# Optimization experiments

Hardware: AMD Instinct MI355X
Metric: run time of the kernel (lower is better)

## Reference

```python
import jax, jax.numpy as jnp
import numpy as np

B, P, H = 256, 20, 4  # images, boxes per image, humans per image
F, L, S, HD, C = 1024, 300, 16, 1024, 117

def _build_edges():
    s, d = np.meshgrid(np.arange(P), np.arange(P), indexing='ij')
    m = s != d
    src_l, dst_l = s[m], d[m]  # 380 fully-connected edges per image (src-major order)
    eid_tab = -np.ones((P, P), np.int64)
    eid_tab[src_l, dst_l] = np.arange(src_l.shape[0])
    rs, rd = np.meshgrid(np.arange(P), np.arange(H), indexing='ij')
    rm = rs != rd
    r_eid = eid_tab[rs[rm], rd[rm]]  # 76 readout edges per image (human dst)
    off_n = (np.arange(B) * P)[:, None]
    off_e = (np.arange(B) * src_l.shape[0])[:, None]
    edge_src = (src_l[None] + off_n).ravel().astype(np.int32)
    edge_dst = (dst_l[None] + off_n).ravel().astype(np.int32)
    readout_eid = (r_eid[None] + off_e).ravel().astype(np.int32)
    return edge_src, edge_dst, readout_eid

def setup_inputs() -> dict:
    key = jax.random.key(0)
    ks = jax.random.split(key, 12)
    es, ed, re = _build_edges()
    N = B * P
    D_in = 2 * F + 2 * L + S  # 2664
    return {
        'feat': jax.random.normal(ks[0], (N, F), jnp.float32),
        'word2vec': jax.random.normal(ks[1], (N, L), jnp.float32),
        'spatial_feat': jax.random.normal(ks[2], (es.shape[0], S), jnp.float32),
        'W_v': jax.random.normal(ks[3], (F, F), jnp.float32) / np.float32(np.sqrt(F)),
        'a_v': jax.random.normal(ks[4], (2 * F,), jnp.float32) * 0.05,
        'W_l': jax.random.normal(ks[5], (L, L), jnp.float32) / np.float32(np.sqrt(L)),
        'a_l': jax.random.normal(ks[6], (2 * L,), jnp.float32) * 0.05,
        'W1': jax.random.normal(ks[7], (D_in, HD), jnp.float32) / np.float32(np.sqrt(D_in)),
        'b1': jnp.zeros((HD,), jnp.float32),
        'W2': jax.random.normal(ks[8], (HD, C), jnp.float32) / np.float32(np.sqrt(HD)),
        'b2': jnp.zeros((C,), jnp.float32),
        'edge_src': jnp.asarray(es),
        'edge_dst': jnp.asarray(ed),
        'readout_eid': jnp.asarray(re),
    }

def _gat_update(x, W, a, src, dst, n):
    # graph-attention message passing (GRNN step): attention over incoming edges per dst
    h = x @ W                      # [N, d]
    d = h.shape[1]
    e_src = h @ a[:d]              # [N]
    e_dst = h @ a[d:]
    e = jax.nn.leaky_relu(e_src[src] + e_dst[dst], 0.2)          # [E]
    emax = jax.ops.segment_max(e, dst, num_segments=n)
    ee = jnp.exp(e - emax[dst])
    denom = jax.ops.segment_sum(ee, dst, num_segments=n)
    alpha = ee / (denom[dst] + 1e-9)                              # segment softmax
    msg = jax.ops.segment_sum(alpha[:, None] * h[src], dst, num_segments=n)  # [N, d]
    return jax.nn.relu(x + msg)

def reference(feat, word2vec, spatial_feat, W_v, a_v, W_l, a_l, W1, b1, W2, b2,
              edge_src, edge_dst, readout_eid):
    n = feat.shape[0]
    new_n_f = _gat_update(feat, W_v, a_v, edge_src, edge_dst, n)          # visual stream
    new_n_f_lang = _gat_update(word2vec, W_l, a_l, edge_src, edge_dst, n) # semantic stream
    s = edge_src[readout_eid]
    d = edge_dst[readout_eid]
    s_f = spatial_feat[readout_eid]
    # Predictor.forward: concat [dst visual, dst lang, edge spatial, src lang, src visual]
    x = jnp.concatenate([new_n_f[d], new_n_f_lang[d], s_f, new_n_f_lang[s], new_n_f[s]], axis=1)
    hdn = jax.nn.relu(x @ W1 + b1)
    return hdn @ W2 + b2  # [Er, 117] action logits
```

## Files before the change

kernel.cpp:

```cpp
#include <hip/hip_runtime.h>
#include <hip/hip_bf16.h>

#define BB 256
#define PP 20
#define HH 4
#define FF 1024
#define LL 300
#define LLP 320
#define DCAT 1344
#define SS 16
#define HDIM 1024
#define CC 117
#define NNODE (BB * PP)
#define NREAD (BB * (PP * HH - HH))
#define EPB 8
#define TK 32

typedef __attribute__((ext_vector_type(8))) short bf16x8v;
typedef __attribute__((ext_vector_type(4))) float f32x4v;
typedef __attribute__((ext_vector_type(4))) unsigned short u16x4;

__device__ __forceinline__ float bf2f(unsigned short u) {
  return __uint_as_float((unsigned int)u << 16);
}
__device__ __forceinline__ unsigned short f2b(float f) {
  __hip_bfloat16 h = __float2bfloat16(f);
  return *(unsigned short*)&h;
}

__global__ void sniff_dtype(const unsigned short* __restrict__ buf,
                            int* __restrict__ flag) {
  int t = threadIdx.x;
  int votes = 0;
  for (int i = t; i < 512; i += 256) {
    unsigned int u = (unsigned int)buf[i] << 16;
    float v = __uint_as_float(u);
    float a = fabsf(v);
    if (v == v && a > 9.3e-10f && a < 1.1e9f) votes++;
  }
  __shared__ int sv[256];
  sv[t] = votes;
  __syncthreads();
  for (int s = 128; s > 0; s >>= 1) {
    if (t < s) sv[t] += sv[t + s];
    __syncthreads();
  }
  if (t == 0) flag[0] = (sv[0] < 448) ? 1 : 0;
}

__global__ __launch_bounds__(256) void convert_strided4(
    const void* __restrict__ src, __hip_bfloat16* __restrict__ dst, int R,
    int C, int ld, int Cp, int dstld, const int* __restrict__ flag) {
  const int cp4 = Cp >> 2;
  long i = (long)blockIdx.x * 256 + threadIdx.x;
  if (i >= (long)R * cp4) return;
  int r = (int)(i / cp4), c = (int)(i % cp4) * 4;
  u16x4 o;
  if (flag[0]) {
    if (c + 4 <= C) {
      float4 v = *(const float4*)((const float*)src + (long)r * ld + c);
      o[0] = f2b(v.x); o[1] = f2b(v.y); o[2] = f2b(v.z); o[3] = f2b(v.w);
    } else {
#pragma unroll
      for (int j = 0; j < 4; j++)
        o[j] = (c + j < C) ? f2b(((const float*)src)[(long)r * ld + c + j]) : 0;
    }
  } else {
    const __hip_bfloat16* s = (const __hip_bfloat16*)src;
    if (c + 4 <= C) {
      o = *(const u16x4*)(s + (long)r * ld + c);
    } else {
#pragma unroll
      for (int j = 0; j < 4; j++) {
        unsigned short u = 0;
        if (c + j < C) u = *(const unsigned short*)(s + (long)r * ld + c + j);
        o[j] = u;
      }
    }
  }
  *(u16x4*)(dst + (long)r * dstld + c) = o;
}

__global__ __launch_bounds__(256) void convert_smalls(
    const void* __restrict__ s4, const void* __restrict__ s6,
    const void* __restrict__ s7, const void* __restrict__ s8,
    const void* __restrict__ s10, __hip_bfloat16* __restrict__ cAv,
    __hip_bfloat16* __restrict__ cAl, __hip_bfloat16* __restrict__ cB1,
    __hip_bfloat16* __restrict__ cB2, __hip_bfloat16* __restrict__ cW1sp,
    const int* __restrict__ flag) {
  int i = blockIdx.x * 256 + threadIdx.x;
  const int f = flag[0];
  auto rd = [&](const void* p, long idx) -> float {
    return f ? ((const float*)p)[idx]
             : __bfloat162float(((const __hip_bfloat16*)p)[idx]);
  };
  if (i < 2048) cAv[i] = __float2bfloat16(rd(s4, i));
  else if (i < 2648) cAl[i - 2048] = __float2bfloat16(rd(s6, i - 2048));
  else if (i < 3672) cB1[i - 2648] = __float2bfloat16(rd(s8, i - 2648));
  else if (i < 3789) cB2[i - 3672] = __float2bfloat16(rd(s10, i - 3672));
  else if (i < 20173)
    cW1sp[i - 3789] = __float2bfloat16(rd(s7, 1355776L + (i - 3789)));
}

__global__ __launch_bounds__(256) void transpose_all(
    const void* __restrict__ s3, const void* __restrict__ s5,
    const void* __restrict__ s7, const void* __restrict__ s9,
    __hip_bfloat16* __restrict__ dWvT, __hip_bfloat16* __restrict__ dWlT,
    __hip_bfloat16* __restrict__ dW1d, __hip_bfloat16* __restrict__ dW1s,
    __hip_bfloat16* __restrict__ dW2T, const int* __restrict__ flag) {
  const int z = blockIdx.z;
  const int ROW0[7] = {0, 0, 0, 1024, 1640, 1340, 0};
  const int KK[7]   = {1024, 300, 1024, 300, 1024, 300, 1024};
  const int NN[7]   = {1024, 300, 1024, 1024, 1024, 1024, 117};
  const int LD[7]   = {1024, 300, 1024, 1024, 1024, 1024, 117};
  const int KP[7]   = {1024, 320, 1024, 320, 1024, 320, 1024};
  const int KOFF[7] = {0, 0, 0, 1024, 0, 1024, 0};
  const int KLD[7]  = {1024, 320, DCAT, DCAT, DCAT, DCAT, 1024};
  const void* src = (z == 0) ? s3 : (z == 1) ? s5 : (z == 6) ? s9 : s7;
  __hip_bfloat16* dst = (z == 0) ? dWvT : (z == 1) ? dWlT
                        : (z <= 3) ? dW1d : (z <= 5) ? dW1s : dW2T;
  const int row0 = ROW0[z], K = KK[z], N = NN[z], ld = LD[z], Kp = KP[z];
  const int koff = KOFF[z], kld = KLD[z];
  const int kb = blockIdx.x * 32, nb = blockIdx.y * 32;
  if (kb >= Kp || nb >= N) return;
  __shared__ float tile[32][33];
  const int tx = threadIdx.x & 31, ty = threadIdx.x >> 5;
  const int fl = flag[0];
  for (int i = ty; i < 32; i += 8) {
    int k = kb + i, n = nb + tx;
    float v = 0.f;
    if (k < K && n < N) {
      long idx = (long)(row0 + k) * ld + n;
      v = fl ? ((const float*)src)[idx]
             : __bfloat162float(((const __hip_bfloat16*)src)[idx]);
    }
    tile[i][tx] = v;
  }
  __syncthreads();
  for (int i = ty; i < 32; i += 8) {
    int n = nb + i, k = kb + tx;
    if (n < N && k < Kp)
      dst[(long)n * kld + koff + k] = __float2bfloat16(tile[tx][i]);
  }
}

struct GDesc {
  const __hip_bfloat16* A;
  const __hip_bfloat16* BT;
  void* C;
  const __hip_bfloat16* bias;
  int M, N, K, lda, ldbt, ldc;
  int row_mode, do_relu, c_mode, nbx, nby;
};

template <int BM, int BN, int WR, int WC>
__global__ __launch_bounds__(256) void gemm_db(GDesc d0, GDesc d1,
                                               const int* outflag) {
  constexpr int MI = BM / WR / 16;
  constexpr int NI = BN / WC / 16;
  __shared__ __hip_bfloat16 Asm[2][BM * TK];
  __shared__ __hip_bfloat16 Bsm[2][BN * TK];
  const GDesc d = blockIdx.z ? d1 : d0;
  if ((int)blockIdx.x >= d.nbx || (int)blockIdx.y >= d.nby) return;
  const int tid = threadIdx.x;
  const int lane = tid & 63;
  const int wave = tid >> 6;
  const int wm = (wave % WR) * (BM / WR);
  const int wn = (wave / WR) * (BN / WC);
  const int m0 = blockIdx.y * BM;
  const int n0 = blockIdx.x * BN;
  const int col_l = lane & 15;
  const int quad = lane >> 4;
  const __hip_bfloat16* A = d.A;
  const __hip_bfloat16* BT = d.BT;
  const int M = d.M, N = d.N, lda = d.lda, ldbt = d.ldbt;
  const int row_mode = d.row_mode;

  auto stage = [&](int k0, int buf) {
#pragma unroll
    for (int p = 0; p < BM / 64; p++) {
      int c = tid + p * 256;
      int r = c >> 2;
      int koff = (c & 3) * 8;
      int row = m0 + r;
      if (row >= M) row = M - 1;
      long grow = row_mode ? ((long)(row >> 2) * PP + (row & 3)) : (long)row;
      const __hip_bfloat16* gp = A + grow * lda + k0 + koff;
      __builtin_amdgcn_global_load_lds(
          (const __attribute__((address_space(1))) unsigned int*)gp,
          (__attribute__((address_space(3))) unsigned int*)(&Asm[buf][c * 8]),
          16, 0, 0);
    }
#pragma unroll
    for (int p = 0; p < BN / 64; p++) {
      int c = tid + p * 256;
      int r = c >> 2;
      int koff = (c & 3) * 8;
      int row = n0 + r;
      if (row >= N) row = N - 1;
      const __hip_bfloat16* gp = BT + (long)row * ldbt + k0 + koff;
      __builtin_amdgcn_global_load_lds(
          (const __attribute__((address_space(1))) unsigned int*)gp,
          (__attribute__((address_space(3))) unsigned int*)(&Bsm[buf][c * 8]),
          16, 0, 0);
    }
  };

  f32x4v acc[MI][NI];
#pragma unroll
  for (int i = 0; i < MI; i++)
#pragma unroll
    for (int j = 0; j < NI; j++)
#pragma unroll
      for (int r = 0; r < 4; r++) acc[i][j][r] = 0.f;

  const int nk = d.K / TK;
  stage(0, 0);
  __syncthreads();
  for (int kt = 0; kt < nk; kt++) {
    const int cur = kt & 1;
    if (kt + 1 < nk) stage((kt + 1) * TK, 1 - cur);
    bf16x8v af[MI], bfr[NI];
#pragma unroll
    for (int mi = 0; mi < MI; mi++)
      af[mi] =
          *(const bf16x8v*)&Asm[cur][(wm + mi * 16 + col_l) * TK + quad * 8];
#pragma unroll
    for (int ni = 0; ni < NI; ni++)
      bfr[ni] =
          *(const bf16x8v*)&Bsm[cur][(wn + ni * 16 + col_l) * TK + quad * 8];
#pragma unroll
    for (int mi = 0; mi < MI; mi++)
#pragma unroll
      for (int ni = 0; ni < NI; ni++)
        acc[mi][ni] = __builtin_amdgcn_mfma_f32_16x16x32_bf16(
            af[mi], bfr[ni], acc[mi][ni], 0, 0, 0);
    __syncthreads();
  }

  const int store_f32 =
      (d.c_mode == 1) || (d.c_mode == 2 && outflag && outflag[0]);
#pragma unroll
  for (int mi = 0; mi < MI; mi++) {
    int rbase = m0 + wm + mi * 16 + quad * 4;
#pragma unroll
    for (int ni = 0; ni < NI; ni++) {
      int col = n0 + wn + ni * 16 + col_l;
      if (col >= N) continue;
      float bv = d.bias ? __bfloat162float(d.bias[col]) : 0.f;
#pragma unroll
      for (int r = 0; r < 4; r++) {
        int row = rbase + r;
        if (row >= M) continue;
        float v = acc[mi][ni][r] + bv;
        if (d.do_relu) v = fmaxf(v, 0.f);
        if (store_f32)
          ((float*)d.C)[(long)row * d.ldc + col] = v;
        else
          ((__hip_bfloat16*)d.C)[(long)row * d.ldc + col] = __float2bfloat16(v);
      }
    }
  }
}

#define CHROW (DCAT / 4)

__global__ __launch_bounds__(1024) void attn_fused(
    const __hip_bfloat16* __restrict__ xcat,
    const __hip_bfloat16* __restrict__ hcat,
    const __hip_bfloat16* __restrict__ aV,
    const __hip_bfloat16* __restrict__ aL,
    __hip_bfloat16* __restrict__ newcat) {
  const int b = blockIdx.x;
  const int t = threadIdx.x;
  const long base = (long)b * PP * DCAT;

  __shared__ __hip_bfloat16 hs[PP][DCAT];
  __shared__ float esv[PP], edv[PP], esl[PP], edl[PP];
  __shared__ float alphaV[PP * PP], alphaL[PP * PP];

  for (int i = t; i < PP * CHROW; i += 1024) {
    int r = i / CHROW, c = (i % CHROW) * 4;
    *(u16x4*)&hs[r][c] = *(const u16x4*)(hcat + base + (long)r * DCAT + c);
  }
  __syncthreads();

  const int wave = t >> 6, lane = t & 63;
  for (int node = wave; node < PP; node += 16) {
    float s1 = 0.f, s2 = 0.f, s3 = 0.f, s4 = 0.f;
    for (int f = lane * 4; f < FF; f += 256) {
      u16x4 hv = *(const u16x4*)&hs[node][f];
      u16x4 a1 = *(const u16x4*)(aV + f);
      u16x4 a2 = *(const u16x4*)(aV + FF + f);
#pragma unroll
      for (int j = 0; j < 4; j++) {
        float hf = bf2f(hv[j]);
        s1 += hf * bf2f(a1[j]);
        s2 += hf * bf2f(a2[j]);
      }
    }
    for (int f = FF + lane * 4; f < FF + LL; f += 256) {
      u16x4 hv = *(const u16x4*)&hs[node][f];
      u16x4 a3 = *(const u16x4*)(aL + (f - FF));
      u16x4 a4 = *(const u16x4*)(aL + LL + (f - FF));
#pragma unroll
      for (int j = 0; j < 4; j++) {
        float hf = bf2f(hv[j]);
        s3 += hf * bf2f(a3[j]);
        s4 += hf * bf2f(a4[j]);
      }
    }
#pragma unroll
    for (int o = 32; o > 0; o >>= 1) {
      s1 += __shfl_down(s1, o);
      s2 += __shfl_down(s2, o);
      s3 += __shfl_down(s3, o);
      s4 += __shfl_down(s4, o);
    }
    if (lane == 0) {
      esv[node] = s1; edv[node] = s2; esl[node] = s3; edl[node] = s4;
    }
  }
  __syncthreads();

  if (t < 2 * PP) {
    const int strm = t / PP, dd = t % PP;
    const float* es = strm ? esl : esv;
    const float ed = strm ? edl[dd] : edv[dd];
    float lg[PP];
    float m = -1e30f;
#pragma unroll
    for (int s = 0; s < PP; s++) {
      float e;
      if (s == dd) e = -1e30f;
      else {
        float v = es[s] + ed;
        e = (v > 0.f) ? v : 0.2f * v;
      }
      lg[s] = e;
      m = fmaxf(m, e);
    }
    float sum = 0.f;
#pragma unroll
    for (int s = 0; s < PP; s++) {
      lg[s] = expf(lg[s] - m);
      sum += lg[s];
    }
    float inv = 1.f / (sum + 1e-9f);
    float* al = strm ? alphaL : alphaV;
#pragma unroll
    for (int s = 0; s < PP; s++) al[s * PP + dd] = lg[s] * inv;
  }
  __syncthreads();

  for (int i = t; i < PP * CHROW; i += 1024) {
    int dd = i / CHROW, c = (i % CHROW) * 4;
    u16x4 ov;
    if (c >= FF + LL) {
      ov[0] = 0; ov[1] = 0; ov[2] = 0; ov[3] = 0;
    } else {
      const float* al = (c < FF) ? (alphaV + dd) : (alphaL + dd);
      float a0 = 0.f, a1 = 0.f, a2 = 0.f, a3 = 0.f;
#pragma unroll
      for (int s = 0; s < PP; s++) {
        float w = al[s * PP];
        u16x4 hv = *(const u16x4*)&hs[s][c];
        a0 += w * bf2f(hv[0]);
        a1 += w * bf2f(hv[1]);
        a2 += w * bf2f(hv[2]);
        a3 += w * bf2f(hv[3]);
      }
      u16x4 xv = *(const u16x4*)(xcat + base + (long)dd * DCAT + c);
      ov[0] = f2b(fmaxf(bf2f(xv[0]) + a0, 0.f));
      ov[1] = f2b(fmaxf(bf2f(xv[1]) + a1, 0.f));
      ov[2] = f2b(fmaxf(bf2f(xv[2]) + a2, 0.f));
      ov[3] = f2b(fmaxf(bf2f(xv[3]) + a3, 0.f));
    }
    *(u16x4*)(newcat + base + (long)dd * DCAT + c) = ov;
  }
}

__global__ __launch_bounds__(256) void combine_kernel(
    const int* __restrict__ e_src, const int* __restrict__ e_dst,
    const int* __restrict__ r_eid, const void* __restrict__ spat_raw,
    const __hip_bfloat16* __restrict__ W1sp,
    const __hip_bfloat16* __restrict__ b1,
    const __hip_bfloat16* __restrict__ Yd, const __hip_bfloat16* __restrict__ Ys,
    __hip_bfloat16* __restrict__ hdn, const int* __restrict__ flag) {
  const int t = threadIdx.x;
  const int e0 = blockIdx.x * EPB;
  const int hd = t * 4;

  float w[SS][4];
#pragma unroll
  for (int k = 0; k < SS; k++) {
    u16x4 ww = *(const u16x4*)(W1sp + (long)k * HDIM + hd);
#pragma unroll
    for (int j = 0; j < 4; j++) w[k][j] = bf2f(ww[j]);
  }
  float bb[4];
  {
    u16x4 bv = *(const u16x4*)(b1 + hd);
#pragma unroll
    for (int j = 0; j < 4; j++) bb[j] = bf2f(bv[j]);
  }

  __shared__ int sh_s[EPB], sh_hx[EPB], sh_re[EPB];
  __shared__ float sh_sf[EPB][SS];
  if (t < EPB) {
    int re = r_eid[e0 + t];
    sh_re[t] = re;
    sh_s[t] = e_src[re];
    int d = e_dst[re];
    sh_hx[t] = (d / PP) * HH + (d % PP);
  }
  __syncthreads();
  if (t < EPB * SS) {
    int ee = t >> 4, k = t & 15;
    long idx = (long)sh_re[ee] * SS + k;
    sh_sf[ee][k] = flag[0]
                       ? ((const float*)spat_raw)[idx]
                       : __bfloat162float(((const __hip_bfloat16*)spat_raw)[idx]);
  }
  __syncthreads();

#pragma unroll
  for (int ee = 0; ee < EPB; ee++) {
    const int s = sh_s[ee];
    const int hx = sh_hx[ee];
    u16x4 yd = *(const u16x4*)(Yd + (long)hx * HDIM + hd);
    u16x4 ys = *(const u16x4*)(Ys + (long)s * HDIM + hd);
    float v[4];
#pragma unroll
    for (int j = 0; j < 4; j++) v[j] = bf2f(yd[j]) + bf2f(ys[j]) + bb[j];
#pragma unroll
    for (int k = 0; k < SS; k++) {
      float sfv = sh_sf[ee][k];
#pragma unroll
      for (int j = 0; j < 4; j++) v[j] += sfv * w[k][j];
    }
    u16x4 o;
#pragma unroll
    for (int j = 0; j < 4; j++) o[j] = f2b(fmaxf(v[j], 0.f));
    *(u16x4*)(hdn + (long)(e0 + ee) * HDIM + hd) = o;
  }
}

extern "C" void kernel_launch(void* const* d_in, const int* in_sizes, int n_in,
                              void* d_out, int out_size, void* d_ws,
                              size_t ws_size, hipStream_t stream) {
  const int* e_src = (const int*)d_in[11];
  const int* e_dst = (const int*)d_in[12];
  const int* r_eid = (const int*)d_in[13];
  (void)ws_size; (void)n_in; (void)in_sizes; (void)out_size;

  char* ws = (char*)d_ws;
  size_t off = 0;
  auto take = [&](size_t bytes) {
    char* p = ws + off;
    off += (bytes + 255) & ~(size_t)255;
    return p;
  };

  int* dflag = (int*)take(256);
  __hip_bfloat16* xcat   = (__hip_bfloat16*)take((size_t)NNODE * DCAT * 2);
  __hip_bfloat16* hcat   = (__hip_bfloat16*)take((size_t)NNODE * DCAT * 2);
  __hip_bfloat16* newcat = (__hip_bfloat16*)take((size_t)NNODE * DCAT * 2);
  __hip_bfloat16* cAv    = (__hip_bfloat16*)take((size_t)2 * FF * 2);
  __hip_bfloat16* cAl    = (__hip_bfloat16*)take((size_t)2 * LL * 2);
  __hip_bfloat16* cB1    = (__hip_bfloat16*)take((size_t)HDIM * 2);
  __hip_bfloat16* cB2    = (__hip_bfloat16*)take((size_t)CC * 2);
  __hip_bfloat16* cW1sp  = (__hip_bfloat16*)take((size_t)SS * HDIM * 2);
  __hip_bfloat16* WvT    = (__hip_bfloat16*)take((size_t)FF * FF * 2);
  __hip_bfloat16* WlT    = (__hip_bfloat16*)take((size_t)LL * LLP * 2);
  __hip_bfloat16* W1Td   = (__hip_bfloat16*)take((size_t)HDIM * DCAT * 2);
  __hip_bfloat16* W1Ts   = (__hip_bfloat16*)take((size_t)HDIM * DCAT * 2);
  __hip_bfloat16* W2T    = (__hip_bfloat16*)take((size_t)CC * HDIM * 2);
  __hip_bfloat16* Yd     = (__hip_bfloat16*)take((size_t)BB * HH * HDIM * 2);
  __hip_bfloat16* Ys     = (__hip_bfloat16*)take((size_t)NNODE * HDIM * 2);
  __hip_bfloat16* hdn    = (__hip_bfloat16*)take((size_t)NREAD * HDIM * 2);

  dim3 blk(256);

  sniff_dtype<<<1, blk, 0, stream>>>((const unsigned short*)d_in[0], dflag);

  {
    long ch = (long)NNODE * (FF / 4);
    convert_strided4<<<(int)((ch + 255) / 256), blk, 0, stream>>>(
        d_in[0], xcat, NNODE, FF, FF, FF, DCAT, dflag);
  }
  {
    long ch = (long)NNODE * (LLP / 4);
    convert_strided4<<<(int)((ch + 255) / 256), blk, 0, stream>>>(
        d_in[1], xcat + FF, NNODE, LL, LL, LLP, DCAT, dflag);
  }
  convert_smalls<<<79, blk, 0, stream>>>(d_in[4], d_in[6], d_in[7], d_in[8],
                                         d_in[10], cAv, cAl, cB1, cB2, cW1sp,
                                         dflag);
  {
    dim3 grid(32, 32, 7);
    transpose_all<<<grid, blk, 0, stream>>>(d_in[3], d_in[5], d_in[7], d_in[9],
                                            WvT, WlT, W1Td, W1Ts, W2T, dflag);
  }

  {
    GDesc pv{xcat, WvT, hcat, nullptr,
             NNODE, FF, FF, DCAT, FF, DCAT, 0, 0, 0, 8, 40};
    GDesc pl{xcat + FF, WlT, hcat + FF, nullptr,
             NNODE, LL, LLP, DCAT, LLP, DCAT, 0, 0, 0, 3, 40};
    gemm_db<128, 128, 2, 2><<<dim3(8, 40, 2), blk, 0, stream>>>(pv, pl,
                                                                nullptr);
  }

  attn_fused<<<BB, dim3(1024), 0, stream>>>(xcat, hcat, cAv, cAl, newcat);

  {
    GDesc gys{newcat, W1Ts, Ys, nullptr,
              NNODE, HDIM, DCAT, DCAT, DCAT, HDIM, 0, 0, 0, 8, 40};
    GDesc gyd{newcat, W1Td, Yd, nullptr,
              BB * HH, HDIM, DCAT, DCAT, DCAT, HDIM, 1, 0, 0, 8, 8};
    gemm_db<128, 128, 2, 2><<<dim3(8, 40, 2), blk, 0, stream>>>(gys, gyd,
                                                                nullptr);
  }

  combine_kernel<<<NREAD / EPB, blk, 0, stream>>>(e_src, e_dst, r_eid, d_in[2],
                                                  cW1sp, cB1, Yd, Ys, hdn,
                                                  dflag);

  {
    GDesc go{hdn, W2T, d_out, cB2,
             NREAD, CC, HDIM, HDIM, HDIM, CC, 0, 0, 2, 1, 304};
    gemm_db<64, 128, 1, 4><<<dim3(1, 304, 1), blk, 0, stream>>>(go, go, dflag);
  }
}
```

Before: 254.9 us.

## Merge prep kernels into one launch and halve GEMM M-tiles for more blocks

Folds the feature/word2vec conversion, small-vector conversion and weight transposes into a single prep_all kernel, indexed by a flat block id, to cut launch overhead. It also shrinks the GEMM tile height (128→64, and 64→32 for the output GEMM) and doubles the grid, so more blocks can fill the CUs. The staging loop is generalized so tiles smaller than 64 rows work. Smaller tiles reduce data reuse per block and add redundant B-tile loads.

```diff
diff --git a/kernel.cpp b/kernel.cpp
--- a/kernel.cpp
+++ b/kernel.cpp
@@ -48,99 +48,116 @@
   if (t == 0) flag[0] = (sv[0] < 448) ? 1 : 0;
 }
 
-__global__ __launch_bounds__(256) void convert_strided4(
-    const void* __restrict__ src, __hip_bfloat16* __restrict__ dst, int R,
-    int C, int ld, int Cp, int dstld, const int* __restrict__ flag) {
-  const int cp4 = Cp >> 2;
-  long i = (long)blockIdx.x * 256 + threadIdx.x;
-  if (i >= (long)R * cp4) return;
-  int r = (int)(i / cp4), c = (int)(i % cp4) * 4;
-  u16x4 o;
-  if (flag[0]) {
-    if (c + 4 <= C) {
-      float4 v = *(const float4*)((const float*)src + (long)r * ld + c);
-      o[0] = f2b(v.x); o[1] = f2b(v.y); o[2] = f2b(v.z); o[3] = f2b(v.w);
-    } else {
-#pragma unroll
-      for (int j = 0; j < 4; j++)
-        o[j] = (c + j < C) ? f2b(((const float*)src)[(long)r * ld + c + j]) : 0;
-    }
-  } else {
-    const __hip_bfloat16* s = (const __hip_bfloat16*)src;
-    if (c + 4 <= C) {
-      o = *(const u16x4*)(s + (long)r * ld + c);
-    } else {
-#pragma unroll
-      for (int j = 0; j < 4; j++) {
-        unsigned short u = 0;
-        if (c + j < C) u = *(const unsigned short*)(s + (long)r * ld + c + j);
-        o[j] = u;
-      }
-    }
-  }
-  *(u16x4*)(dst + (long)r * dstld + c) = o;
-}
-
-__global__ __launch_bounds__(256) void convert_smalls(
-    const void* __restrict__ s4, const void* __restrict__ s6,
+#define NB_FEAT 5120
+#define NB_W2V 1600
+#define NB_SM 79
+#define PREP_BLOCKS 10739
+
+__global__ __launch_bounds__(256) void prep_all(
+    const void* __restrict__ s0, const void* __restrict__ s1,
+    const void* __restrict__ s3, const void* __restrict__ s4,
+    const void* __restrict__ s5, const void* __restrict__ s6,
     const void* __restrict__ s7, const void* __restrict__ s8,
-    const void* __restrict__ s10, __hip_bfloat16* __restrict__ cAv,
+    const void* __restrict__ s9, const void* __restrict__ s10,
+    __hip_bfloat16* __restrict__ xcat, __hip_bfloat16* __restrict__ cAv,
     __hip_bfloat16* __restrict__ cAl, __hip_bfloat16* __restrict__ cB1,
     __hip_bfloat16* __restrict__ cB2, __hip_bfloat16* __restrict__ cW1sp,
-    const int* __restrict__ flag) {
-  int i = blockIdx.x * 256 + threadIdx.x;
-  const int f = flag[0];
-  auto rd = [&](const void* p, long idx) -> float {
-    return f ? ((const float*)p)[idx]
-             : __bfloat162float(((const __hip_bfloat16*)p)[idx]);
-  };
-  if (i < 2048) cAv[i] = __float2bfloat16(rd(s4, i));
-  else if (i < 2648) cAl[i - 2048] = __float2bfloat16(rd(s6, i - 2048));
-  else if (i < 3672) cB1[i - 2648] = __float2bfloat16(rd(s8, i - 2648));
-  else if (i < 3789) cB2[i - 3672] = __float2bfloat16(rd(s10, i - 3672));
-  else if (i < 20173)
-    cW1sp[i - 3789] = __float2bfloat16(rd(s7, 1355776L + (i - 3789)));
-}
-
-__global__ __launch_bounds__(256) void transpose_all(
-    const void* __restrict__ s3, const void* __restrict__ s5,
-    const void* __restrict__ s7, const void* __restrict__ s9,
     __hip_bfloat16* __restrict__ dWvT, __hip_bfloat16* __restrict__ dWlT,
     __hip_bfloat16* __restrict__ dW1d, __hip_bfloat16* __restrict__ dW1s,
     __hip_bfloat16* __restrict__ dW2T, const int* __restrict__ flag) {
-  const int z = blockIdx.z;
-  const int ROW0[7] = {0, 0, 0, 1024, 1640, 1340, 0};
-  const int KK[7]   = {1024, 300, 1024, 300, 1024, 300, 1024};
-  const int NN[7]   = {1024, 300, 1024, 1024, 1024, 1024, 117};
-  const int LD[7]   = {1024, 300, 1024, 1024, 1024, 1024, 117};
-  const int KP[7]   = {1024, 320, 1024, 320, 1024, 320, 1024};
-  const int KOFF[7] = {0, 0, 0, 1024, 0, 1024, 0};
-  const int KLD[7]  = {1024, 320, DCAT, DCAT, DCAT, DCAT, 1024};
-  const void* src = (z == 0) ? s3 : (z == 1) ? s5 : (z == 6) ? s9 : s7;
-  __hip_bfloat16* dst = (z == 0) ? dWvT : (z == 1) ? dWlT
-                        : (z <= 3) ? dW1d : (z <= 5) ? dW1s : dW2T;
-  const int row0 = ROW0[z], K = KK[z], N = NN[z], ld = LD[z], Kp = KP[z];
-  const int koff = KOFF[z], kld = KLD[z];
-  const int kb = blockIdx.x * 32, nb = blockIdx.y * 32;
-  if (kb >= Kp || nb >= N) return;
-  __shared__ float tile[32][33];
-  const int tx = threadIdx.x & 31, ty = threadIdx.x >> 5;
+  const int bid = blockIdx.x;
+  const int t = threadIdx.x;
   const int fl = flag[0];
-  for (int i = ty; i < 32; i += 8) {
-    int k = kb + i, n = nb + tx;
-    float v = 0.f;
-    if (k < K && n < N) {
-      long idx = (long)(row0 + k) * ld + n;
-      v = fl ? ((const float*)src)[idx]
-             : __bfloat162float(((const __hip_bfloat16*)src)[idx]);
-    }
-    tile[i][tx] = v;
-  }
-  __syncthreads();
-  for (int i = ty; i < 32; i += 8) {
-    int n = nb + i, k = kb + tx;
-    if (n < N && k < Kp)
-      dst[(long)n * kld + koff + k] = __float2bfloat16(tile[tx][i]);
+
+  if (bid < NB_FEAT) {
+    long i = (long)bid * 256 + t;
+    int r = (int)(i >> 8);
+    int c = ((int)i & 255) * 4;
+    u16x4 o;
+    if (fl) {
+      float4 v = *(const float4*)((const float*)s0 + (long)r * FF + c);
+      o[0] = f2b(v.x); o[1] = f2b(v.y); o[2] = f2b(v.z); o[3] = f2b(v.w);
+    } else {
+      o = *(const u16x4*)((const __hip_bfloat16*)s0 + (long)r * FF + c);
+    }
+    *(u16x4*)(xcat + (long)r * DCAT + c) = o;
+  } else if (bid < NB_FEAT + NB_W2V) {
+    long i = (long)(bid - NB_FEAT) * 256 + t;
+    int r = (int)(i / 80), c = ((int)(i % 80)) * 4;
+    u16x4 o;
+    if (c + 4 <= LL) {
+      if (fl) {
+        const float* p = (const float*)s1 + (long)r * LL + c;
+        o[0] = f2b(p[0]); o[1] = f2b(p[1]); o[2] = f2b(p[2]); o[3] = f2b(p[3]);
+      } else {
+        const __hip_bfloat16* p = (const __hip_bfloat16*)s1 + (long)r * LL + c;
+        o[0] = *(const unsigned short*)(p + 0);
+        o[1] = *(const unsigned short*)(p + 1);
+        o[2] = *(const unsigned short*)(p + 2);
+        o[3] = *(const unsigned short*)(p + 3);
+      }
+    } else {
+#pragma unroll
+      for (int j = 0; j < 4; j++) {
+        float v = 0.f;
+        if (c + j < LL)
+          v = fl ? ((const float*)s1)[(long)r * LL + c + j]
+                 : __bfloat162float(
+                       ((const __hip_bfloat16*)s1)[(long)r * LL + c + j]);
+        o[j] = f2b(v);
+      }
+    }
+    *(u16x4*)(xcat + (long)r * DCAT + FF + c) = o;
+  } else if (bid < NB_FEAT + NB_W2V + NB_SM) {
+    int i = (bid - NB_FEAT - NB_W2V) * 256 + t;
+    auto rd = [&](const void* p, long idx) -> float {
+      return fl ? ((const float*)p)[idx]
+                : __bfloat162float(((const __hip_bfloat16*)p)[idx]);
+    };
+    if (i < 2048) cAv[i] = __float2bfloat16(rd(s4, i));
+    else if (i < 2648) cAl[i - 2048] = __float2bfloat16(rd(s6, i - 2048));
+    else if (i < 3672) cB1[i - 2648] = __float2bfloat16(rd(s8, i - 2648));
+    else if (i < 3789) cB2[i - 3672] = __float2bfloat16(rd(s10, i - 3672));
+    else if (i < 20173)
+      cW1sp[i - 3789] = __float2bfloat16(rd(s7, 1355776L + (i - 3789)));
+  } else {
+    int idx = bid - (NB_FEAT + NB_W2V + NB_SM);
+    const int OFFS[8] = {0, 1024, 1124, 2148, 2468, 3492, 3812, 3940};
+    const int NKB[7] = {32, 10, 32, 10, 32, 10, 32};
+    const int ROW0[7] = {0, 0, 0, 1024, 1640, 1340, 0};
+    const int KK[7] = {1024, 300, 1024, 300, 1024, 300, 1024};
+    const int NN[7] = {1024, 300, 1024, 1024, 1024, 1024, 117};
+    const int LD[7] = {1024, 300, 1024, 1024, 1024, 1024, 117};
+    const int KP[7] = {1024, 320, 1024, 320, 1024, 320, 1024};
+    const int KOFF[7] = {0, 0, 0, 1024, 0, 1024, 0};
+    const int KLD[7] = {1024, 320, DCAT, DCAT, DCAT, DCAT, 1024};
+    int z = 0;
+    while (z < 6 && idx >= OFFS[z + 1]) z++;
+    idx -= OFFS[z];
+    const int kb = (idx % NKB[z]) * 32, nb = (idx / NKB[z]) * 32;
+    const void* src = (z == 0) ? s3 : (z == 1) ? s5 : (z == 6) ? s9 : s7;
+    __hip_bfloat16* dst = (z == 0) ? dWvT : (z == 1) ? dWlT
+                          : (z <= 3) ? dW1d : (z <= 5) ? dW1s : dW2T;
+    const int row0 = ROW0[z], K = KK[z], N = NN[z], ld = LD[z], Kp = KP[z];
+    const int koff = KOFF[z], kld = KLD[z];
+    __shared__ float tile[32][33];
+    const int tx = t & 31, ty = t >> 5;
+    for (int i = ty; i < 32; i += 8) {
+      int k = kb + i, n = nb + tx;
+      float v = 0.f;
+      if (k < K && n < N) {
+        long sidx = (long)(row0 + k) * ld + n;
+        v = fl ? ((const float*)src)[sidx]
+               : __bfloat162float(((const __hip_bfloat16*)src)[sidx]);
+      }
+      tile[i][tx] = v;
+    }
+    __syncthreads();
+    for (int i = ty; i < 32; i += 8) {
+      int n = nb + i, k = kb + tx;
+      if (n < N && k < Kp)
+        dst[(long)n * kld + koff + k] = __float2bfloat16(tile[tx][i]);
+    }
   }
 }
 
@@ -178,8 +195,7 @@
 
   auto stage = [&](int k0, int buf) {
 #pragma unroll
-    for (int p = 0; p < BM / 64; p++) {
-      int c = tid + p * 256;
+    for (int c = tid; c < BM * 4; c += 256) {
       int r = c >> 2;
       int koff = (c & 3) * 8;
       int row = m0 + r;
@@ -192,8 +208,7 @@
           16, 0, 0);
     }
 #pragma unroll
-    for (int p = 0; p < BN / 64; p++) {
-      int c = tid + p * 256;
+    for (int c = tid; c < BN * 4; c += 256) {
       int r = c >> 2;
       int koff = (c & 3) * 8;
       int row = n0 + r;
@@ -484,43 +499,29 @@
 
   sniff_dtype<<<1, blk, 0, stream>>>((const unsigned short*)d_in[0], dflag);
 
-  {
-    long ch = (long)NNODE * (FF / 4);
-    convert_strided4<<<(int)((ch + 255) / 256), blk, 0, stream>>>(
-        d_in[0], xcat, NNODE, FF, FF, FF, DCAT, dflag);
-  }
-  {
-    long ch = (long)NNODE * (LLP / 4);
-    convert_strided4<<<(int)((ch + 255) / 256), blk, 0, stream>>>(
-        d_in[1], xcat + FF, NNODE, LL, LL, LLP, DCAT, dflag);
-  }
-  convert_smalls<<<79, blk, 0, stream>>>(d_in[4], d_in[6], d_in[7], d_in[8],
-                                         d_in[10], cAv, cAl, cB1, cB2, cW1sp,
-                                         dflag);
-  {
-    dim3 grid(32, 32, 7);
-    transpose_all<<<grid, blk, 0, stream>>>(d_in[3], d_in[5], d_in[7], d_in[9],
-                                            WvT, WlT, W1Td, W1Ts, W2T, dflag);
-  }
+  prep_all<<<PREP_BLOCKS, blk, 0, stream>>>(
+      d_in[0], d_in[1], d_in[3], d_in[4], d_in[5], d_in[6], d_in[7], d_in[8],
+      d_in[9], d_in[10], xcat, cAv, cAl, cB1, cB2, cW1sp, WvT, WlT, W1Td, W1Ts,
+      W2T, dflag);
 
   {
     GDesc pv{xcat, WvT, hcat, nullptr,
-             NNODE, FF, FF, DCAT, FF, DCAT, 0, 0, 0, 8, 40};
+             NNODE, FF, FF, DCAT, FF, DCAT, 0, 0, 0, 8, 80};
     GDesc pl{xcat + FF, WlT, hcat + FF, nullptr,
-             NNODE, LL, LLP, DCAT, LLP, DCAT, 0, 0, 0, 3, 40};
-    gemm_db<128, 128, 2, 2><<<dim3(8, 40, 2), blk, 0, stream>>>(pv, pl,
-                                                                nullptr);
+             NNODE, LL, LLP, DCAT, LLP, DCAT, 0, 0, 0, 3, 80};
+    gemm_db<64, 128, 2, 2><<<dim3(8, 80, 2), blk, 0, stream>>>(pv, pl,
+                                                               nullptr);
   }
 
   attn_fused<<<BB, dim3(1024), 0, stream>>>(xcat, hcat, cAv, cAl, newcat);
 
   {
     GDesc gys{newcat, W1Ts, Ys, nullptr,
-              NNODE, HDIM, DCAT, DCAT, DCAT, HDIM, 0, 0, 0, 8, 40};
+              NNODE, HDIM, DCAT, DCAT, DCAT, HDIM, 0, 0, 0, 8, 80};
     GDesc gyd{newcat, W1Td, Yd, nullptr,
-              BB * HH, HDIM, DCAT, DCAT, DCAT, HDIM, 1, 0, 0, 8, 8};
-    gemm_db<128, 128, 2, 2><<<dim3(8, 40, 2), blk, 0, stream>>>(gys, gyd,
-                                                                nullptr);
+              BB * HH, HDIM, DCAT, DCAT, DCAT, HDIM, 1, 0, 0, 8, 16};
+    gemm_db<64, 128, 2, 2><<<dim3(8, 80, 2), blk, 0, stream>>>(gys, gyd,
+                                                               nullptr);
   }
 
   combine_kernel<<<NREAD / EPB, blk, 0, stream>>>(e_src, e_dst, r_eid, d_in[2],
@@ -529,7 +530,7 @@
 
   {
     GDesc go{hdn, W2T, d_out, cB2,
-             NREAD, CC, HDIM, HDIM, HDIM, CC, 0, 0, 2, 1, 304};
-    gemm_db<64, 128, 1, 4><<<dim3(1, 304, 1), blk, 0, stream>>>(go, go, dflag);
-  }
-}
+             NREAD, CC, HDIM, HDIM, HDIM, CC, 0, 0, 2, 1, 608};
+    gemm_db<32, 128, 1, 4><<<dim3(1, 608, 1), blk, 0, stream>>>(go, go, dflag);
+  }
+}
```

New measurement: 246.7 us. -3.2%, faster.
